# Kernel optimization log

Hardware: AMD Instinct MI355X
Metric: run time of the kernel (lower is better)

Reference implementation:

```python
import jax, jax.numpy as jnp
import numpy as np

N = 20000          # num_nodes
E = 160000         # directed edges (doubled to undirected inside reference)
NF, EF, H, OUT, K = 16, 16, 128, 16, 3


def mlp2(x, w1, b1, w2, b2):
    return jnp.maximum(x @ w1 + b1, 0.0) @ w2 + b2


def edge_agg(x, src, dst, eattr, w1, b1, w2, b2):
    # message = MLP(cat[x_i (target), x_j (source), edge_attr]); aggr='add' at target
    m = mlp2(jnp.concatenate([x[dst], x[src], eattr], axis=-1), w1, b1, w2, b2)
    return jax.ops.segment_sum(m, dst, num_segments=x.shape[0])


def tag_conv(x, src, dst, lins, bias):
    # PyG TAGConv: gcn_norm (no self loops), out = sum_k lin_k(L^k x) + bias
    n = x.shape[0]
    deg = jax.ops.segment_sum(jnp.ones_like(src, dtype=x.dtype), dst, num_segments=n)
    dis = jnp.where(deg > 0, jax.lax.rsqrt(deg), 0.0)
    norm = dis[src] * dis[dst]                     # [E]
    out = x @ lins[0]
    h = x
    for k in range(1, lins.shape[0]):
        h = jax.ops.segment_sum(norm[:, None] * h[src], dst, num_segments=n)
        out = out + h @ lins[k]
    return out + bias


def setup_inputs() -> dict:
    key = jax.random.key(0)
    ks = jax.random.split(key, 20)
    s = 0.05
    lin = lambda k, i, o: jax.random.normal(k, (i, o), jnp.float32) * s
    inp = {}
    inp["x"] = jax.random.normal(ks[0], (N, NF), jnp.float32)
    inp["mask"] = (jax.random.uniform(ks[1], (N, NF)) > 0.5).astype(jnp.float32)
    inp["edge_attr"] = jax.random.normal(ks[2], (E, EF), jnp.float32)
    inp["edge_index"] = jax.random.randint(ks[3], (2, E), 0, N)
    inp["m_w1"] = lin(ks[4], NF, H); inp["m_b1"] = jnp.zeros(H)
    inp["m_w2"] = lin(ks[5], H, NF); inp["m_b2"] = jnp.zeros(NF)
    inp["ea0_w1"] = lin(ks[6], 2 * NF + EF, H); inp["ea0_b1"] = jnp.zeros(H)
    inp["ea0_w2"] = lin(ks[7], H, H); inp["ea0_b2"] = jnp.zeros(H)
    inp["tag0_w"] = jax.random.normal(ks[8], (K + 1, H, H), jnp.float32) * s
    inp["tag0_b"] = jnp.zeros(H)
    inp["ea1_w1"] = lin(ks[9], 2 * H + EF, H); inp["ea1_b1"] = jnp.zeros(H)
    inp["ea1_w2"] = lin(ks[10], H, H); inp["ea1_b2"] = jnp.zeros(H)
    inp["tag1_w"] = jax.random.normal(ks[11], (K + 1, H, H), jnp.float32) * s
    inp["tag1_b"] = jnp.zeros(H)
    inp["ea2_w1"] = lin(ks[12], 2 * H + EF, H); inp["ea2_b1"] = jnp.zeros(H)
    inp["ea2_w2"] = lin(ks[13], H, OUT); inp["ea2_b2"] = jnp.zeros(OUT)
    return inp


def reference(x, mask, edge_attr, m_w1, m_b1, m_w2, m_b2,
              ea0_w1, ea0_b1, ea0_w2, ea0_b2, tag0_w, tag0_b,
              ea1_w1, ea1_b1, ea1_w2, ea1_b2, tag1_w, tag1_b,
              ea2_w1, ea2_b1, ea2_w2, ea2_b2, edge_index):
    # undirect_graph: random directed edges -> duplicate reversed copies
    src0, dst0 = edge_index[0], edge_index[1]
    src = jnp.concatenate([src0, dst0])
    dst = jnp.concatenate([dst0, src0])
    ea = jnp.concatenate([edge_attr, edge_attr], axis=0)
    # mask embedding + residual
    h = mlp2(mask, m_w1, m_b1, m_w2, m_b2) + x
    # [EA, TAG, EA, TAG] with ReLU (dropout = identity in eval)
    h = jnp.maximum(edge_agg(h, src, dst, ea, ea0_w1, ea0_b1, ea0_w2, ea0_b2), 0.0)
    h = jnp.maximum(tag_conv(h, src, dst, tag0_w, tag0_b), 0.0)
    h = jnp.maximum(edge_agg(h, src, dst, ea, ea1_w1, ea1_b1, ea1_w2, ea1_b2), 0.0)
    h = jnp.maximum(tag_conv(h, src, dst, tag1_w, tag1_b), 0.0)
    # final EA (no activation)
    return edge_agg(h, src, dst, ea, ea2_w1, ea2_b1, ea2_w2, ea2_b2)
```

## Files before the change

kernel.cpp:

```cpp
#include <hip/hip_runtime.h>

typedef unsigned short u16;
typedef unsigned int u32;

using bfrag  = __attribute__((ext_vector_type(8))) short;
using f32x4  = __attribute__((ext_vector_type(4))) float;
using f32x16 = __attribute__((ext_vector_type(16))) float;

__device__ __forceinline__ float b2f(u16 u) {
  union { u32 i; float f; } c; c.i = ((u32)u) << 16; return c.f;
}
__device__ __forceinline__ float bflo(u32 u) { union { u32 i; float f; } c; c.i = u << 16; return c.f; }
__device__ __forceinline__ float bfhi(u32 u) { union { u32 i; float f; } c; c.i = u & 0xffff0000u; return c.f; }
__device__ __forceinline__ u16 f2b(float f) {
  union { float f; u32 i; } c; c.f = f;
  u32 x = c.i;
  u32 r = x + 0x7fffu + ((x >> 16) & 1u);
  return (u16)(r >> 16);
}
__device__ __forceinline__ u32 packb2(float x, float y) {
  return ((u32)f2b(x)) | (((u32)f2b(y)) << 16);
}
__device__ __forceinline__ u16 f2h(float x) {
  union { _Float16 h; u16 u; } c; c.h = (_Float16)x; return c.u;
}
__device__ __forceinline__ float h2lo(u32 u) { union { u32 i; _Float16 h[2]; } c; c.i = u; return (float)c.h[0]; }
__device__ __forceinline__ float h2hi(u32 u) { union { u32 i; _Float16 h[2]; } c; c.i = u; return (float)c.h[1]; }
__device__ __forceinline__ int rfl(int v) { return __builtin_amdgcn_readfirstlane(v); }

__global__ __launch_bounds__(256) void count_deg(const int* __restrict__ eidx,
                                                 int* __restrict__ degi, int E) {
  int e = blockIdx.x * 256 + threadIdx.x;
  if (e >= E) return;
  atomicAdd(&degi[eidx[E + e]], 1);
  atomicAdd(&degi[eidx[e]], 1);
}

__global__ __launch_bounds__(256) void scan1(const int* __restrict__ degi,
                                             int* __restrict__ bsum, int N) {
  __shared__ int sh[256];
  int t = threadIdx.x;
  int gid = blockIdx.x * 256 + t;
  sh[t] = (gid < N) ? degi[gid] : 0;
  __syncthreads();
  for (int off = 128; off > 0; off >>= 1) {
    if (t < off) sh[t] += sh[t + off];
    __syncthreads();
  }
  if (t == 0) bsum[blockIdx.x] = sh[0];
}

__global__ __launch_bounds__(256) void scan2(int* __restrict__ bsum,
                                             int* __restrict__ rowptr, int nb, int N) {
  __shared__ int sh[256];
  int t = threadIdx.x;
  int v = (t < nb) ? bsum[t] : 0;
  sh[t] = v;
  __syncthreads();
  for (int off = 1; off < 256; off <<= 1) {
    int x = sh[t];
    int add = (t >= off) ? sh[t - off] : 0;
    __syncthreads();
    sh[t] = x + add;
    __syncthreads();
  }
  if (t < nb) bsum[t] = sh[t] - v;
  if (t == nb - 1) rowptr[N] = sh[t];
}

__global__ __launch_bounds__(256) void scan3(const int* __restrict__ degi,
                                             const int* __restrict__ bsum,
                                             int* __restrict__ rowptr,
                                             int* __restrict__ cursor,
                                             float* __restrict__ dis, int N) {
  __shared__ int sh[256];
  int t = threadIdx.x;
  int gid = blockIdx.x * 256 + t;
  int d = (gid < N) ? degi[gid] : 0;
  sh[t] = d;
  __syncthreads();
  for (int off = 1; off < 256; off <<= 1) {
    int x = sh[t];
    int add = (t >= off) ? sh[t - off] : 0;
    __syncthreads();
    sh[t] = x + add;
    __syncthreads();
  }
  if (gid < N) {
    int run = bsum[blockIdx.x] + sh[t] - d;
    rowptr[gid] = run;
    cursor[gid] = run;
    dis[gid] = d > 0 ? rsqrtf((float)d) : 0.0f;
  }
}

__global__ __launch_bounds__(256) void fill_csr(const int* __restrict__ eidx,
                                                int* __restrict__ cursor,
                                                const float* __restrict__ dis,
                                                int2* __restrict__ cw,
                                                int2* __restrict__ ce, int E) {
  int i = blockIdx.x * 256 + threadIdx.x;
  int E2 = 2 * E;
  if (i >= E2) return;
  int e = (i < E) ? i : i - E;
  int s, d;
  if (i < E) { s = eidx[e]; d = eidx[E + e]; }
  else       { s = eidx[E + e]; d = eidx[e]; }
  int pos = atomicAdd(&cursor[d], 1);
  cw[pos] = make_int2(s, __float_as_int(dis[s]));
  ce[pos] = make_int2(s, e);
}

__global__ __launch_bounds__(256) void prep_wt(
    const float* __restrict__ ea0_w2, const float* __restrict__ tag0_w,
    const float* __restrict__ ea1_w1, const float* __restrict__ ea1_w2,
    const float* __restrict__ tag1_w, const float* __restrict__ ea2_w1,
    const float* __restrict__ ea0_w1,
    u16* __restrict__ Wt, u16* __restrict__ W3, int* __restrict__ degi, int N) {
  int gid = blockIdx.x * 256 + threadIdx.x;
  if (gid < N) degi[gid] = 0;
  int t = threadIdx.x;
  if (blockIdx.x >= 112) {
    int tab = blockIdx.x - 112;
    const float* src = (tab == 0) ? (ea0_w1 + 32 * 128)
                     : (tab == 1) ? (ea1_w1 + 256 * 128)
                                  : (ea2_w1 + 256 * 128);
    u16* dst = W3 + tab * 2048;
    for (int i = 0; i < 8; ++i) {
      int idx = i * 256 + t;
      int n = idx >> 4, k = idx & 15;
      dst[idx] = f2b(src[k * 128 + n]);
    }
    return;
  }
  int mat = blockIdx.x >> 3, chunk = blockIdx.x & 7;
  const float* src;
  if      (mat == 0)  src = ea0_w2;
  else if (mat <= 4)  src = tag0_w + (mat - 1) * 16384;
  else if (mat == 5)  src = ea1_w1;
  else if (mat == 6)  src = ea1_w1 + 16384;
  else if (mat == 7)  src = ea1_w2;
  else if (mat <= 11) src = tag1_w + (mat - 8) * 16384;
  else if (mat == 12) src = ea2_w1;
  else                src = ea2_w1 + 16384;
  u16* dst = Wt + mat * 16384;
  for (int i = 0; i < 8; ++i) {
    int idx = chunk * 2048 + i * 256 + t;
    int k = idx >> 7, n = idx & 127;
    dst[n * 128 + k] = f2b(src[idx]);
  }
}

__global__ __launch_bounds__(256) void ea_proj_mfma(
    const float* __restrict__ ea, const u16* __restrict__ W3,
    u16* __restrict__ P0, u16* __restrict__ P1, u16* __restrict__ P2, int E) {
  __shared__ u16 Alds[64 * 16];
  __shared__ u16 Wlds[3 * 2048];
  int t = threadIdx.x;
  int base = blockIdx.x * 64;
  int rows = E - base; if (rows > 64) rows = 64;
#pragma unroll
  for (int i = 0; i < 3; ++i)
    *(uint4*)(Wlds + (i * 256 + t) * 8) = *(const uint4*)(W3 + (i * 256 + t) * 8);
#pragma unroll
  for (int i = 0; i < 4; ++i) {
    int idx = (i * 256 + t) * 4;
    float4 v = make_float4(0.f, 0.f, 0.f, 0.f);
    if ((idx >> 4) < rows) v = *(const float4*)(ea + (size_t)base * 16 + idx);
    ushort4 h;
    h.x = f2b(v.x); h.y = f2b(v.y); h.z = f2b(v.z); h.w = f2b(v.w);
    *(ushort4*)(Alds + idx) = h;
  }
  __syncthreads();
  int wave = t >> 6, lane = t & 63;
  int rowt = (wave >> 1) * 32;
  int colt = (wave & 1) * 64;
  int mm = lane & 31, kh = lane >> 5;
  bfrag a = *(const bfrag*)(Alds + (rowt + mm) * 16 + kh * 8);
#pragma unroll
  for (int tab = 0; tab < 3; ++tab) {
    const u16* wl = Wlds + tab * 2048;
    bfrag b0 = *(const bfrag*)(wl + (colt + mm) * 16 + kh * 8);
    bfrag b1 = *(const bfrag*)(wl + (colt + 32 + mm) * 16 + kh * 8);
    f32x16 acc0, acc1;
#pragma unroll
    for (int z = 0; z < 16; ++z) { acc0[z] = 0.f; acc1[z] = 0.f; }
    acc0 = __builtin_amdgcn_mfma_f32_32x32x16_bf16(a, b0, acc0, 0, 0, 0);
    acc1 = __builtin_amdgcn_mfma_f32_32x32x16_bf16(a, b1, acc1, 0, 0, 0);
    u16* P = (tab == 0) ? P0 : (tab == 1) ? P1 : P2;
#pragma unroll
    for (int reg = 0; reg < 16; ++reg) {
      int row = rowt + (reg & 3) + 8 * (reg >> 2) + 4 * kh;
      if (row < rows) {
        size_t off = (size_t)(base + row) * 128;
        P[off + colt + mm]      = f2h(acc0[reg]);
        P[off + colt + 32 + mm] = f2h(acc1[reg]);
      }
    }
  }
}

__global__ __launch_bounds__(128) void gemm_head(
    const float* __restrict__ mask, const float* __restrict__ x,
    const float* __restrict__ m_w1, const float* __restrict__ m_b1,
    const float* __restrict__ m_w2, const float* __restrict__ m_b2,
    const float* __restrict__ ea0_w1, const float* __restrict__ ea0_b1,
    u16* __restrict__ pb, u16* __restrict__ q, int M) {
  const int ROWS = 8;
  int t = threadIdx.x;
  int base = blockIdx.x * ROWS;
  __shared__ float Ml[ROWS * 16];
  __shared__ float T1[ROWS * 128];
  __shared__ float H[ROWS * 16];
  for (int i = t; i < ROWS * 16; i += 128) {
    int r = i >> 4, k = i & 15;
    int row = base + r;
    Ml[i] = (row < M) ? mask[(size_t)row * 16 + k] : 0.f;
  }
  __syncthreads();
  {
    float acc[ROWS];
#pragma unroll
    for (int r = 0; r < ROWS; ++r) acc[r] = m_b1[t];
    for (int k = 0; k < 16; ++k) {
      float w = m_w1[k * 128 + t];
#pragma unroll
      for (int r = 0; r < ROWS; ++r) acc[r] += Ml[r * 16 + k] * w;
    }
#pragma unroll
    for (int r = 0; r < ROWS; ++r) T1[r * 128 + t] = fmaxf(acc[r], 0.f);
  }
  __syncthreads();
  {
    int r = t >> 4, u = t & 15;
    float acc = m_b2[u];
    for (int k = 0; k < 128; ++k) acc += T1[r * 128 + k] * m_w2[k * 16 + u];
    int row = base + r;
    float xv = (row < M) ? x[(size_t)row * 16 + u] : 0.f;
    H[r * 16 + u] = acc + xv;
  }
  __syncthreads();
  {
    float aP[ROWS], aQ[ROWS];
    float b1v = ea0_b1[t];
#pragma unroll
    for (int r = 0; r < ROWS; ++r) { aP[r] = b1v; aQ[r] = 0.f; }
    for (int k = 0; k < 16; ++k) {
      float wd = ea0_w1[k * 128 + t];
      float ws = ea0_w1[(16 + k) * 128 + t];
#pragma unroll
      for (int r = 0; r < ROWS; ++r) {
        float h = H[r * 16 + k];
        aP[r] += h * wd;
        aQ[r] += h * ws;
      }
    }
#pragma unroll
    for (int r = 0; r < ROWS; ++r) {
      int row = base + r;
      if (row < M) {
        pb[(size_t)row * 128 + t] = f2b(aP[r]);
        q[(size_t)row * 128 + t]  = f2b(aQ[r]);
      }
    }
  }
}

template<bool OUTBF16>
__global__ __launch_bounds__(256) void gemm_mfma(
    const u16* __restrict__ A, const u16* __restrict__ Wt,
    void* __restrict__ Cout, const float* __restrict__ bias,
    const int* __restrict__ degi, int M, int relu) {
  __shared__ u16 Alds[64 * 136];
  __shared__ u16 Wlds[128 * 136];
  int t = threadIdx.x;
  int base = blockIdx.x * 64;
#pragma unroll
  for (int i = 0; i < 8; ++i) {
    int idx = (i * 256 + t) * 8;
    int n = idx >> 7, k = idx & 127;
    uint4 v = *(const uint4*)(Wt + idx);
    *(uint4*)(Wlds + n * 136 + k) = v;
  }
#pragma unroll
  for (int i = 0; i < 4; ++i) {
    int idx = (i * 256 + t) * 8;
    int r = idx >> 7, k = idx & 127;
    int row = base + r;
    uint4 v = make_uint4(0, 0, 0, 0);
    if (row < M) v = *(const uint4*)(A + (size_t)row * 128 + k);
    *(uint4*)(Alds + r * 136 + k) = v;
  }
  __syncthreads();
  int wave = t >> 6, lane = t & 63;
  int m = lane & 15, quad = lane >> 4;
  int arow = wave * 16 + m;
  bfrag a[4];
#pragma unroll
  for (int ks = 0; ks < 4; ++ks)
    a[ks] = *(const bfrag*)(Alds + arow * 136 + ks * 32 + quad * 8);
  f32x4 acc[8];
#pragma unroll
  for (int nt = 0; nt < 8; ++nt) acc[nt] = (f32x4){0.f, 0.f, 0.f, 0.f};
#pragma unroll
  for (int nt = 0; nt < 8; ++nt) {
    int n = nt * 16 + m;
#pragma unroll
    for (int ks = 0; ks < 4; ++ks) {
      bfrag b = *(const bfrag*)(Wlds + n * 136 + ks * 32 + quad * 8);
      acc[nt] = __builtin_amdgcn_mfma_f32_16x16x32_bf16(a[ks], b, acc[nt], 0, 0, 0);
    }
  }
#pragma unroll
  for (int nt = 0; nt < 8; ++nt) {
    int col = nt * 16 + m;
#pragma unroll
    for (int r = 0; r < 4; ++r) {
      int row = base + wave * 16 + quad * 4 + r;
      if (row < M) {
        float v = acc[nt][r];
        if (bias) { float b = bias[col]; v += degi ? b * (float)degi[row] : b; }
        if (relu) v = fmaxf(v, 0.f);
        if (OUTBF16) ((u16*)Cout)[(size_t)row * 128 + col] = f2b(v);
        else         ((float*)Cout)[(size_t)row * 128 + col] = v;
      }
    }
  }
}

__global__ __launch_bounds__(256) void gemm_mfma_dual(
    const u16* __restrict__ A, const u16* __restrict__ W0t, const u16* __restrict__ W1t,
    u16* __restrict__ C0, u16* __restrict__ C1, const float* __restrict__ bias0, int M) {
  __shared__ u16 Alds[64 * 136];
  __shared__ u16 Wlds[128 * 136];
  int t = threadIdx.x;
  int base = blockIdx.x * 64;
#pragma unroll
  for (int i = 0; i < 8; ++i) {
    int idx = (i * 256 + t) * 8;
    int n = idx >> 7, k = idx & 127;
    uint4 v = *(const uint4*)(W0t + idx);
    *(uint4*)(Wlds + n * 136 + k) = v;
  }
#pragma unroll
  for (int i = 0; i < 4; ++i) {
    int idx = (i * 256 + t) * 8;
    int r = idx >> 7, k = idx & 127;
    int row = base + r;
    uint4 v = make_uint4(0, 0, 0, 0);
    if (row < M) v = *(const uint4*)(A + (size_t)row * 128 + k);
    *(uint4*)(Alds + r * 136 + k) = v;
  }
  __syncthreads();
  int wave = t >> 6, lane = t & 63;
  int m = lane & 15, quad = lane >> 4;
  int arow = wave * 16 + m;
  bfrag a[4];
#pragma unroll
  for (int ks = 0; ks < 4; ++ks)
    a[ks] = *(const bfrag*)(Alds + arow * 136 + ks * 32 + quad * 8);
  f32x4 acc0[8], acc1[8];
#pragma unroll
  for (int nt = 0; nt < 8; ++nt) { acc0[nt] = (f32x4){0,0,0,0}; acc1[nt] = (f32x4){0,0,0,0}; }
#pragma unroll
  for (int nt = 0; nt < 8; ++nt) {
    int n = nt * 16 + m;
#pragma unroll
    for (int ks = 0; ks < 4; ++ks) {
      bfrag b = *(const bfrag*)(Wlds + n * 136 + ks * 32 + quad * 8);
      acc0[nt] = __builtin_amdgcn_mfma_f32_16x16x32_bf16(a[ks], b, acc0[nt], 0, 0, 0);
    }
  }
  __syncthreads();
#pragma unroll
  for (int i = 0; i < 8; ++i) {
    int idx = (i * 256 + t) * 8;
    int n = idx >> 7, k = idx & 127;
    uint4 v = *(const uint4*)(W1t + idx);
    *(uint4*)(Wlds + n * 136 + k) = v;
  }
  __syncthreads();
#pragma unroll
  for (int nt = 0; nt < 8; ++nt) {
    int n = nt * 16 + m;
#pragma unroll
    for (int ks = 0; ks < 4; ++ks) {
      bfrag b = *(const bfrag*)(Wlds + n * 136 + ks * 32 + quad * 8);
      acc1[nt] = __builtin_amdgcn_mfma_f32_16x16x32_bf16(a[ks], b, acc1[nt], 0, 0, 0);
    }
  }
#pragma unroll
  for (int nt = 0; nt < 8; ++nt) {
    int col = nt * 16 + m;
#pragma unroll
    for (int r = 0; r < 4; ++r) {
      int row = base + wave * 16 + quad * 4 + r;
      if (row < M) {
        float v0 = acc0[nt][r];
        if (bias0) v0 += bias0[col];
        C0[(size_t)row * 128 + col] = f2b(v0);
        C1[(size_t)row * 128 + col] = f2b(acc1[nt][r]);
      }
    }
  }
}

__global__ __launch_bounds__(256) void gemm_mfma_quad(
    const u16* __restrict__ A, const u16* __restrict__ Wt4,
    u16* __restrict__ G0, u16* __restrict__ G1,
    u16* __restrict__ G2, u16* __restrict__ G3, int M) {
  __shared__ u16 Alds[64 * 136];
  __shared__ u16 Wlds[128 * 136];
  int t = threadIdx.x;
  int base = blockIdx.x * 64;
#pragma unroll
  for (int i = 0; i < 4; ++i) {
    int idx = (i * 256 + t) * 8;
    int r = idx >> 7, k = idx & 127;
    int row = base + r;
    uint4 v = make_uint4(0, 0, 0, 0);
    if (row < M) v = *(const uint4*)(A + (size_t)row * 128 + k);
    *(uint4*)(Alds + r * 136 + k) = v;
  }
  __syncthreads();
  int wave = t >> 6, lane = t & 63;
  int m = lane & 15, quad = lane >> 4;
  int arow = wave * 16 + m;
  bfrag a[4];
#pragma unroll
  for (int ks = 0; ks < 4; ++ks)
    a[ks] = *(const bfrag*)(Alds + arow * 136 + ks * 32 + quad * 8);
#pragma unroll
  for (int mat = 0; mat < 4; ++mat) {
    __syncthreads();
#pragma unroll
    for (int i = 0; i < 8; ++i) {
      int idx = (i * 256 + t) * 8;
      int n = idx >> 7, k = idx & 127;
      uint4 v = *(const uint4*)(Wt4 + mat * 16384 + idx);
      *(uint4*)(Wlds + n * 136 + k) = v;
    }
    __syncthreads();
    f32x4 acc[8];
#pragma unroll
    for (int nt = 0; nt < 8; ++nt) acc[nt] = (f32x4){0.f, 0.f, 0.f, 0.f};
#pragma unroll
    for (int nt = 0; nt < 8; ++nt) {
      int n = nt * 16 + m;
#pragma unroll
      for (int ks = 0; ks < 4; ++ks) {
        bfrag b = *(const bfrag*)(Wlds + n * 136 + ks * 32 + quad * 8);
        acc[nt] = __builtin_amdgcn_mfma_f32_16x16x32_bf16(a[ks], b, acc[nt], 0, 0, 0);
      }
    }
    u16* G = (mat == 0) ? G0 : (mat == 1) ? G1 : (mat == 2) ? G2 : G3;
#pragma unroll
    for (int nt = 0; nt < 8; ++nt) {
      int col = nt * 16 + m;
#pragma unroll
      for (int r = 0; r < 4; ++r) {
        int row = base + wave * 16 + quad * 4 + r;
        if (row < M) G[(size_t)row * 128 + col] = f2b(acc[nt][r]);
      }
    }
  }
}

__global__ __launch_bounds__(128) void gemm_tail(
    const u16* __restrict__ A, const float* __restrict__ W, float* __restrict__ Cout,
    const float* __restrict__ bias, const int* __restrict__ degi, int M) {
  const int ROWS = 8;
  int t = threadIdx.x;
  int base = blockIdx.x * ROWS;
  __shared__ float Al[ROWS * 128];
  for (int i = t; i < ROWS * 128; i += 128) {
    int r = i >> 7, k = i & 127;
    int row = base + r;
    Al[i] = (row < M) ? b2f(A[(size_t)row * 128 + k]) : 0.f;
  }
  __syncthreads();
  int r = t >> 4, u = t & 15;
  int row = base + r;
  float acc = 0.f;
  for (int k = 0; k < 128; ++k) acc += Al[r * 128 + k] * W[k * 16 + u];
  if (row < M) {
    Cout[(size_t)row * 16 + u] = acc + bias[u] * (float)degi[row];
  }
}

__device__ __forceinline__ void tag_edge(const int2* __restrict__ rr, int j,
    const u16* __restrict__ g, int lane, float& x0, float& x1) {
  int2 r = rr[j];
  int s = rfl(r.x); float w = __uint_as_float(rfl(r.y));
  u32 h = *((const u32*)(g + (size_t)s * 128) + lane);
  x0 += w * bflo(h); x1 += w * bfhi(h);
}
__device__ __forceinline__ void ea_edge(const int2* __restrict__ rr, int j,
    const u16* __restrict__ q, const u16* __restrict__ P, int lane,
    float pb0, float pb1, float& x0, float& x1) {
  int2 r = rr[j];
  int s = rfl(r.x), i = rfl(r.y);
  u32 qv = *((const u32*)(q + (size_t)s * 128) + lane);
  u32 pv = *((const u32*)(P + (size_t)i * 128) + lane);
  x0 += fmaxf(pb0 + bflo(qv) + h2lo(pv), 0.f);
  x1 += fmaxf(pb1 + bfhi(qv) + h2hi(pv), 0.f);
}

template<bool FINAL>
__global__ __launch_bounds__(256) void tag_gather8(
    const u16* __restrict__ g, const u16* __restrict__ Cin,
    const float* __restrict__ bias, const float* __restrict__ dis,
    const int* __restrict__ rowptr, const int2* __restrict__ cw,
    u16* __restrict__ out, int N) {
  __shared__ int2 recs[4][64];
  int wave = threadIdx.x >> 6, lane = threadIdx.x & 63;
  int node = blockIdx.x * 4 + wave;
  if (node >= N) return;
  int e0 = rfl(rowptr[node]);
  int e1 = rfl(rowptr[node + 1]);
  int2* rr = recs[wave];
  float a0 = 0, a1 = 0, b0 = 0, b1 = 0;
  for (int base = e0; base < e1; base += 64) {
    if (base + lane < e1) rr[lane] = cw[base + lane];
    int cnt = min(64, e1 - base);
    int j = 0;
    for (; j + 8 <= cnt; j += 8) {
      tag_edge(rr, j + 0, g, lane, a0, a1);
      tag_edge(rr, j + 1, g, lane, b0, b1);
      tag_edge(rr, j + 2, g, lane, a0, a1);
      tag_edge(rr, j + 3, g, lane, b0, b1);
      tag_edge(rr, j + 4, g, lane, a0, a1);
      tag_edge(rr, j + 5, g, lane, b0, b1);
      tag_edge(rr, j + 6, g, lane, a0, a1);
      tag_edge(rr, j + 7, g, lane, b0, b1);
    }
    for (; j + 2 <= cnt; j += 2) {
      tag_edge(rr, j + 0, g, lane, a0, a1);
      tag_edge(rr, j + 1, g, lane, b0, b1);
    }
    if (j < cnt) tag_edge(rr, j, g, lane, a0, a1);
  }
  float dn = dis[node];
  float r0v = dn * (a0 + b0), r1v = dn * (a1 + b1);
  u32 cin = *((const u32*)(Cin + (size_t)node * 128) + lane);
  r0v += bflo(cin); r1v += bfhi(cin);
  if (FINAL) {
    float2 bv = *(const float2*)(bias + 2 * lane);
    r0v = fmaxf(r0v + bv.x, 0.f);
    r1v = fmaxf(r1v + bv.y, 0.f);
  }
  *((u32*)(out + (size_t)node * 128) + lane) = packb2(r0v, r1v);
}

__global__ __launch_bounds__(256) void ea_gather8(
    const u16* __restrict__ pb, const u16* __restrict__ q,
    const u16* __restrict__ P ,
    const int* __restrict__ rowptr, const int2* __restrict__ ce,
    u16* __restrict__ Hsum, int N) {
  __shared__ int2 recs[4][64];
  int wave = threadIdx.x >> 6, lane = threadIdx.x & 63;
  int node = blockIdx.x * 4 + wave;
  if (node >= N) return;
  int e0 = rfl(rowptr[node]);
  int e1 = rfl(rowptr[node + 1]);
  int2* rr = recs[wave];
  u32 pbu = *((const u32*)(pb + (size_t)node * 128) + lane);
  float pb0 = bflo(pbu), pb1 = bfhi(pbu);
  float a0 = 0, a1 = 0, b0 = 0, b1 = 0;
  for (int base = e0; base < e1; base += 64) {
    if (base + lane < e1) rr[lane] = ce[base + lane];
    int cnt = min(64, e1 - base);
    int j = 0;
    for (; j + 8 <= cnt; j += 8) {
      ea_edge(rr, j + 0, q, P, lane, pb0, pb1, a0, a1);
      ea_edge(rr, j + 1, q, P, lane, pb0, pb1, b0, b1);
      ea_edge(rr, j + 2, q, P, lane, pb0, pb1, a0, a1);
      ea_edge(rr, j + 3, q, P, lane, pb0, pb1, b0, b1);
      ea_edge(rr, j + 4, q, P, lane, pb0, pb1, a0, a1);
      ea_edge(rr, j + 5, q, P, lane, pb0, pb1, b0, b1);
      ea_edge(rr, j + 6, q, P, lane, pb0, pb1, a0, a1);
      ea_edge(rr, j + 7, q, P, lane, pb0, pb1, b0, b1);
    }
    for (; j + 2 <= cnt; j += 2) {
      ea_edge(rr, j + 0, q, P, lane, pb0, pb1, a0, a1);
      ea_edge(rr, j + 1, q, P, lane, pb0, pb1, b0, b1);
    }
    if (j < cnt) ea_edge(rr, j, q, P, lane, pb0, pb1, a0, a1);
  }
  *((u32*)(Hsum + (size_t)node * 128) + lane) = packb2(a0 + b0, a1 + b1);
}

extern "C" void kernel_launch(void* const* d_in, const int* in_sizes, int n_in,
                              void* d_out, int out_size, void* d_ws, size_t ws_size,
                              hipStream_t stream) {
  const float* x      = (const float*)d_in[0];
  const float* mask   = (const float*)d_in[1];
  const float* ea     = (const float*)d_in[2];
  const int*   eidx   = (const int*)d_in[3];
  const float* m_w1   = (const float*)d_in[4];
  const float* m_b1   = (const float*)d_in[5];
  const float* m_w2   = (const float*)d_in[6];
  const float* m_b2   = (const float*)d_in[7];
  const float* ea0_w1 = (const float*)d_in[8];
  const float* ea0_b1 = (const float*)d_in[9];
  const float* ea0_w2 = (const float*)d_in[10];
  const float* ea0_b2 = (const float*)d_in[11];
  const float* tag0_w = (const float*)d_in[12];
  const float* tag0_b = (const float*)d_in[13];
  const float* ea1_w1 = (const float*)d_in[14];
  const float* ea1_b1 = (const float*)d_in[15];
  const float* ea1_w2 = (const float*)d_in[16];
  const float* ea1_b2 = (const float*)d_in[17];
  const float* tag1_w = (const float*)d_in[18];
  const float* tag1_b = (const float*)d_in[19];
  const float* ea2_w1 = (const float*)d_in[20];
  const float* ea2_b1 = (const float*)d_in[21];
  const float* ea2_w2 = (const float*)d_in[22];
  const float* ea2_b2 = (const float*)d_in[23];

  const int N = in_sizes[0] / 16;
  const int E = in_sizes[2] / 16;
  const int E2 = 2 * E;
  const int NB = (N + 255) / 256;

  char* w = (char*)d_ws;
  auto alloc = [&](size_t bytes) { char* p = w; w += (bytes + 255) & ~(size_t)255; return p; };
  int*   degi   = (int*)alloc((size_t)N * 4);
  int*   cursor = (int*)alloc((size_t)N * 4);
  int*   rowptr = (int*)alloc((size_t)(N + 1) * 4);
  int*   bsum   = (int*)alloc((size_t)256 * 4);
  float* dis    = (float*)alloc((size_t)N * 4);
  int2*  cw     = (int2*)alloc((size_t)E2 * 8);
  int2*  ce     = (int2*)alloc((size_t)E2 * 8);
  u16*   X0     = (u16*)alloc((size_t)N * 128 * 2);
  u16*   X1     = (u16*)alloc((size_t)N * 128 * 2);
  u16*   X2     = (u16*)alloc((size_t)N * 128 * 2);
  u16*   G0     = (u16*)alloc((size_t)N * 128 * 2);
  u16*   G1     = (u16*)alloc((size_t)N * 128 * 2);
  u16*   G2     = (u16*)alloc((size_t)N * 128 * 2);
  u16*   G3     = (u16*)alloc((size_t)N * 128 * 2);
  u16*   Wt     = (u16*)alloc((size_t)14 * 16384 * 2);
  u16*   W3     = (u16*)alloc((size_t)3 * 2048 * 2);
  u16*   P0     = (u16*)alloc((size_t)E * 128 * 2);
  u16*   P1     = (u16*)alloc((size_t)E * 128 * 2);
  u16*   P2     = (u16*)alloc((size_t)E * 128 * 2);
  (void)ws_size; (void)n_in; (void)out_size;

  prep_wt<<<115, 256, 0, stream>>>(ea0_w2, tag0_w, ea1_w1, ea1_w2, tag1_w, ea2_w1,
                                   ea0_w1, Wt, W3, degi, N);
  ea_proj_mfma<<<(E + 63) / 64, 256, 0, stream>>>(ea, W3, P0, P1, P2, E);
  count_deg<<<(E + 255) / 256, 256, 0, stream>>>(eidx, degi, E);
  scan1<<<NB, 256, 0, stream>>>(degi, bsum, N);
  scan2<<<1, 256, 0, stream>>>(bsum, rowptr, NB, N);
  scan3<<<NB, 256, 0, stream>>>(degi, bsum, rowptr, cursor, dis, N);
  fill_csr<<<(E2 + 255) / 256, 256, 0, stream>>>(eidx, cursor, dis, cw, ce, E);

  const int gb = (N + 7) / 8;
  const int gm = (N + 63) / 64;
  const int g4 = (N + 3) / 4;
  u16* WT_ea0w2  = Wt + 0 * 16384;
  u16* WT_tag0   = Wt + 1 * 16384;
  u16* WT_ea1d   = Wt + 5 * 16384;
  u16* WT_ea1s   = Wt + 6 * 16384;
  u16* WT_ea1w2  = Wt + 7 * 16384;
  u16* WT_tag1   = Wt + 8 * 16384;
  u16* WT_ea2d   = Wt + 12 * 16384;
  u16* WT_ea2s   = Wt + 13 * 16384;

  gemm_head<<<gb, 128, 0, stream>>>(mask, x, m_w1, m_b1, m_w2, m_b2,
                                    ea0_w1, ea0_b1, X0, X1, N);

  ea_gather8<<<g4, 256, 0, stream>>>(X0, X1, P0, rowptr, ce, X2, N);
  gemm_mfma<true><<<gm, 256, 0, stream>>>(X2, WT_ea0w2, X0, ea0_b2, degi, N, 1);

  gemm_mfma_quad<<<gm, 256, 0, stream>>>(X0, WT_tag0, G0, G1, G2, G3, N);
  tag_gather8<false><<<g4, 256, 0, stream>>>(G3, G2, nullptr, dis, rowptr, cw, X1, N);
  tag_gather8<false><<<g4, 256, 0, stream>>>(X1, G1, nullptr, dis, rowptr, cw, X2, N);
  tag_gather8<true><<<g4, 256, 0, stream>>>(X2, G0, tag0_b, dis, rowptr, cw, X0, N);

  gemm_mfma_dual<<<gm, 256, 0, stream>>>(X0, WT_ea1d, WT_ea1s, X1, X2, ea1_b1, N);
  ea_gather8<<<g4, 256, 0, stream>>>(X1, X2, P1, rowptr, ce, G0, N);
  gemm_mfma<true><<<gm, 256, 0, stream>>>(G0, WT_ea1w2, X0, ea1_b2, degi, N, 1);

  gemm_mfma_quad<<<gm, 256, 0, stream>>>(X0, WT_tag1, G0, G1, G2, G3, N);
  tag_gather8<false><<<g4, 256, 0, stream>>>(G3, G2, nullptr, dis, rowptr, cw, X1, N);
  tag_gather8<false><<<g4, 256, 0, stream>>>(X1, G1, nullptr, dis, rowptr, cw, X2, N);
  tag_gather8<true><<<g4, 256, 0, stream>>>(X2, G0, tag1_b, dis, rowptr, cw, X0, N);

  gemm_mfma_dual<<<gm, 256, 0, stream>>>(X0, WT_ea2d, WT_ea2s, X1, X2, ea2_b1, N);
  ea_gather8<<<g4, 256, 0, stream>>>(X1, X2, P2, rowptr, ce, G0, N);
  gemm_tail<<<gb, 128, 0, stream>>>(G0, ea2_w2, (float*)d_out, ea2_b2, degi, N);
}
```

Measured before the change: 429.4 us.

## Fuse prologue kernels and merge EA second-layer GEMM into TAG quad GEMM

Merges weight prep, edge-attr projection and degree counting into one prologue launch, merges CSR fill with the head MLP, and fuses the EA w2 GEMM (bias×degree, ReLU) into the TAG four-way GEMM via LDS. The aim is fewer kernel launches and no round trip of the intermediate node features through global memory. In the second penta call G0 is both input and output, which can race across blocks only if tiles overlap. Each block reads its own rows before writing, so it looks safe.

```diff
diff --git a/kernel.cpp b/kernel.cpp
--- a/kernel.cpp
+++ b/kernel.cpp
@@ -28,112 +28,78 @@
 __device__ __forceinline__ float h2hi(u32 u) { union { u32 i; _Float16 h[2]; } c; c.i = u; return (float)c.h[1]; }
 __device__ __forceinline__ int rfl(int v) { return __builtin_amdgcn_readfirstlane(v); }
 
-__global__ __launch_bounds__(256) void count_deg(const int* __restrict__ eidx,
-                                                 int* __restrict__ degi, int E) {
-  int e = blockIdx.x * 256 + threadIdx.x;
-  if (e >= E) return;
-  atomicAdd(&degi[eidx[E + e]], 1);
-  atomicAdd(&degi[eidx[e]], 1);
-}
-
-__global__ __launch_bounds__(256) void scan1(const int* __restrict__ degi,
-                                             int* __restrict__ bsum, int N) {
-  __shared__ int sh[256];
-  int t = threadIdx.x;
-  int gid = blockIdx.x * 256 + t;
-  sh[t] = (gid < N) ? degi[gid] : 0;
-  __syncthreads();
-  for (int off = 128; off > 0; off >>= 1) {
-    if (t < off) sh[t] += sh[t + off];
-    __syncthreads();
-  }
-  if (t == 0) bsum[blockIdx.x] = sh[0];
-}
-
-__global__ __launch_bounds__(256) void scan2(int* __restrict__ bsum,
-                                             int* __restrict__ rowptr, int nb, int N) {
-  __shared__ int sh[256];
-  int t = threadIdx.x;
-  int v = (t < nb) ? bsum[t] : 0;
-  sh[t] = v;
-  __syncthreads();
-  for (int off = 1; off < 256; off <<= 1) {
-    int x = sh[t];
-    int add = (t >= off) ? sh[t - off] : 0;
-    __syncthreads();
-    sh[t] = x + add;
-    __syncthreads();
-  }
-  if (t < nb) bsum[t] = sh[t] - v;
-  if (t == nb - 1) rowptr[N] = sh[t];
-}
-
-__global__ __launch_bounds__(256) void scan3(const int* __restrict__ degi,
-                                             const int* __restrict__ bsum,
-                                             int* __restrict__ rowptr,
-                                             int* __restrict__ cursor,
-                                             float* __restrict__ dis, int N) {
-  __shared__ int sh[256];
-  int t = threadIdx.x;
-  int gid = blockIdx.x * 256 + t;
-  int d = (gid < N) ? degi[gid] : 0;
-  sh[t] = d;
-  __syncthreads();
-  for (int off = 1; off < 256; off <<= 1) {
-    int x = sh[t];
-    int add = (t >= off) ? sh[t - off] : 0;
-    __syncthreads();
-    sh[t] = x + add;
-    __syncthreads();
-  }
-  if (gid < N) {
-    int run = bsum[blockIdx.x] + sh[t] - d;
-    rowptr[gid] = run;
-    cursor[gid] = run;
-    dis[gid] = d > 0 ? rsqrtf((float)d) : 0.0f;
-  }
-}
-
-__global__ __launch_bounds__(256) void fill_csr(const int* __restrict__ eidx,
-                                                int* __restrict__ cursor,
-                                                const float* __restrict__ dis,
-                                                int2* __restrict__ cw,
-                                                int2* __restrict__ ce, int E) {
-  int i = blockIdx.x * 256 + threadIdx.x;
-  int E2 = 2 * E;
-  if (i >= E2) return;
-  int e = (i < E) ? i : i - E;
-  int s, d;
-  if (i < E) { s = eidx[e]; d = eidx[E + e]; }
-  else       { s = eidx[E + e]; d = eidx[e]; }
-  int pos = atomicAdd(&cursor[d], 1);
-  cw[pos] = make_int2(s, __float_as_int(dis[s]));
-  ce[pos] = make_int2(s, e);
-}
-
-__global__ __launch_bounds__(256) void prep_wt(
-    const float* __restrict__ ea0_w2, const float* __restrict__ tag0_w,
-    const float* __restrict__ ea1_w1, const float* __restrict__ ea1_w2,
-    const float* __restrict__ tag1_w, const float* __restrict__ ea2_w1,
-    const float* __restrict__ ea0_w1,
-    u16* __restrict__ Wt, u16* __restrict__ W3, int* __restrict__ degi, int N) {
-  int gid = blockIdx.x * 256 + threadIdx.x;
-  if (gid < N) degi[gid] = 0;
-  int t = threadIdx.x;
-  if (blockIdx.x >= 112) {
-    int tab = blockIdx.x - 112;
-    const float* src = (tab == 0) ? (ea0_w1 + 32 * 128)
-                     : (tab == 1) ? (ea1_w1 + 256 * 128)
-                                  : (ea2_w1 + 256 * 128);
-    u16* dst = W3 + tab * 2048;
+__global__ __launch_bounds__(256) void prologue(
+    const float* __restrict__ ea, const int* __restrict__ eidx,
+    const float* __restrict__ ea0_w1, const float* __restrict__ ea0_w2,
+    const float* __restrict__ tag0_w, const float* __restrict__ ea1_w1,
+    const float* __restrict__ ea1_w2, const float* __restrict__ tag1_w,
+    const float* __restrict__ ea2_w1,
+    u16* __restrict__ P0, u16* __restrict__ P1, u16* __restrict__ P2,
+    int* __restrict__ degi, u16* __restrict__ Wt, int E, int N,
+    int PB, int CB) {
+  int t = threadIdx.x;
+  if (blockIdx.x < (unsigned)PB) {
+    __shared__ u16 Alds[64 * 16];
+    __shared__ u16 Wlds[3 * 2048];
+    int base = blockIdx.x * 64;
+    int rows = E - base; if (rows > 64) rows = 64;
+    const float* wsrc[3] = { ea0_w1 + 32 * 128, ea1_w1 + 256 * 128, ea2_w1 + 256 * 128 };
+#pragma unroll
     for (int i = 0; i < 8; ++i) {
       int idx = i * 256 + t;
       int n = idx >> 4, k = idx & 15;
-      dst[idx] = f2b(src[k * 128 + n]);
+      Wlds[0 * 2048 + idx] = f2b(wsrc[0][k * 128 + n]);
+      Wlds[1 * 2048 + idx] = f2b(wsrc[1][k * 128 + n]);
+      Wlds[2 * 2048 + idx] = f2b(wsrc[2][k * 128 + n]);
+    }
+#pragma unroll
+    for (int i = 0; i < 4; ++i) {
+      int idx = (i * 256 + t) * 4;
+      float4 v = make_float4(0.f, 0.f, 0.f, 0.f);
+      if ((idx >> 4) < rows) v = *(const float4*)(ea + (size_t)base * 16 + idx);
+      ushort4 h;
+      h.x = f2b(v.x); h.y = f2b(v.y); h.z = f2b(v.z); h.w = f2b(v.w);
+      *(ushort4*)(Alds + idx) = h;
+    }
+    __syncthreads();
+    int wave = t >> 6, lane = t & 63;
+    int rowt = (wave >> 1) * 32;
+    int colt = (wave & 1) * 64;
+    int mm = lane & 31, kh = lane >> 5;
+    bfrag a = *(const bfrag*)(Alds + (rowt + mm) * 16 + kh * 8);
+#pragma unroll
+    for (int tab = 0; tab < 3; ++tab) {
+      const u16* wl = Wlds + tab * 2048;
+      bfrag b0 = *(const bfrag*)(wl + (colt + mm) * 16 + kh * 8);
+      bfrag b1 = *(const bfrag*)(wl + (colt + 32 + mm) * 16 + kh * 8);
+      f32x16 acc0, acc1;
+#pragma unroll
+      for (int z = 0; z < 16; ++z) { acc0[z] = 0.f; acc1[z] = 0.f; }
+      acc0 = __builtin_amdgcn_mfma_f32_32x32x16_bf16(a, b0, acc0, 0, 0, 0);
+      acc1 = __builtin_amdgcn_mfma_f32_32x32x16_bf16(a, b1, acc1, 0, 0, 0);
+      u16* P = (tab == 0) ? P0 : (tab == 1) ? P1 : P2;
+#pragma unroll
+      for (int reg = 0; reg < 16; ++reg) {
+        int row = rowt + (reg & 3) + 8 * (reg >> 2) + 4 * kh;
+        if (row < rows) {
+          size_t off = (size_t)(base + row) * 128;
+          P[off + colt + mm]      = f2h(acc0[reg]);
+          P[off + colt + 32 + mm] = f2h(acc1[reg]);
+        }
+      }
     }
     return;
   }
-  int mat = blockIdx.x >> 3, chunk = blockIdx.x & 7;
+  if (blockIdx.x < (unsigned)(PB + CB)) {
+    int e = (blockIdx.x - PB) * 256 + t;
+    if (e < E) {
+      atomicAdd(&degi[eidx[E + e]], 1);
+      atomicAdd(&degi[eidx[e]], 1);
+    }
+    return;
+  }
+  int wb = blockIdx.x - PB - CB;
+  int mat = wb >> 3, chunk = wb & 7;
   const float* src;
   if      (mat == 0)  src = ea0_w2;
   else if (mat <= 4)  src = tag0_w + (mat - 1) * 16384;
@@ -151,84 +117,109 @@
   }
 }
 
-__global__ __launch_bounds__(256) void ea_proj_mfma(
-    const float* __restrict__ ea, const u16* __restrict__ W3,
-    u16* __restrict__ P0, u16* __restrict__ P1, u16* __restrict__ P2, int E) {
-  __shared__ u16 Alds[64 * 16];
-  __shared__ u16 Wlds[3 * 2048];
-  int t = threadIdx.x;
-  int base = blockIdx.x * 64;
-  int rows = E - base; if (rows > 64) rows = 64;
-#pragma unroll
-  for (int i = 0; i < 3; ++i)
-    *(uint4*)(Wlds + (i * 256 + t) * 8) = *(const uint4*)(W3 + (i * 256 + t) * 8);
-#pragma unroll
-  for (int i = 0; i < 4; ++i) {
-    int idx = (i * 256 + t) * 4;
-    float4 v = make_float4(0.f, 0.f, 0.f, 0.f);
-    if ((idx >> 4) < rows) v = *(const float4*)(ea + (size_t)base * 16 + idx);
-    ushort4 h;
-    h.x = f2b(v.x); h.y = f2b(v.y); h.z = f2b(v.z); h.w = f2b(v.w);
-    *(ushort4*)(Alds + idx) = h;
-  }
-  __syncthreads();
-  int wave = t >> 6, lane = t & 63;
-  int rowt = (wave >> 1) * 32;
-  int colt = (wave & 1) * 64;
-  int mm = lane & 31, kh = lane >> 5;
-  bfrag a = *(const bfrag*)(Alds + (rowt + mm) * 16 + kh * 8);
-#pragma unroll
-  for (int tab = 0; tab < 3; ++tab) {
-    const u16* wl = Wlds + tab * 2048;
-    bfrag b0 = *(const bfrag*)(wl + (colt + mm) * 16 + kh * 8);
-    bfrag b1 = *(const bfrag*)(wl + (colt + 32 + mm) * 16 + kh * 8);
-    f32x16 acc0, acc1;
-#pragma unroll
-    for (int z = 0; z < 16; ++z) { acc0[z] = 0.f; acc1[z] = 0.f; }
-    acc0 = __builtin_amdgcn_mfma_f32_32x32x16_bf16(a, b0, acc0, 0, 0, 0);
-    acc1 = __builtin_amdgcn_mfma_f32_32x32x16_bf16(a, b1, acc1, 0, 0, 0);
-    u16* P = (tab == 0) ? P0 : (tab == 1) ? P1 : P2;
-#pragma unroll
-    for (int reg = 0; reg < 16; ++reg) {
-      int row = rowt + (reg & 3) + 8 * (reg >> 2) + 4 * kh;
-      if (row < rows) {
-        size_t off = (size_t)(base + row) * 128;
-        P[off + colt + mm]      = f2h(acc0[reg]);
-        P[off + colt + 32 + mm] = f2h(acc1[reg]);
-      }
-    }
-  }
-}
-
-__global__ __launch_bounds__(128) void gemm_head(
+__global__ __launch_bounds__(256) void scan1(const int* __restrict__ degi,
+                                             int* __restrict__ bsum, int N) {
+  __shared__ int sh[256];
+  int t = threadIdx.x;
+  int gid = blockIdx.x * 256 + t;
+  sh[t] = (gid < N) ? degi[gid] : 0;
+  __syncthreads();
+  for (int off = 128; off > 0; off >>= 1) {
+    if (t < off) sh[t] += sh[t + off];
+    __syncthreads();
+  }
+  if (t == 0) bsum[blockIdx.x] = sh[0];
+}
+
+__global__ __launch_bounds__(256) void scan2(int* __restrict__ bsum,
+                                             int* __restrict__ rowptr, int nb, int N) {
+  __shared__ int sh[256];
+  int t = threadIdx.x;
+  int v = (t < nb) ? bsum[t] : 0;
+  sh[t] = v;
+  __syncthreads();
+  for (int off = 1; off < 256; off <<= 1) {
+    int x = sh[t];
+    int add = (t >= off) ? sh[t - off] : 0;
+    __syncthreads();
+    sh[t] = x + add;
+    __syncthreads();
+  }
+  if (t < nb) bsum[t] = sh[t] - v;
+  if (t == nb - 1) rowptr[N] = sh[t];
+}
+
+__global__ __launch_bounds__(256) void scan3(const int* __restrict__ degi,
+                                             const int* __restrict__ bsum,
+                                             int* __restrict__ rowptr,
+                                             int* __restrict__ cursor,
+                                             float* __restrict__ dis, int N) {
+  __shared__ int sh[256];
+  int t = threadIdx.x;
+  int gid = blockIdx.x * 256 + t;
+  int d = (gid < N) ? degi[gid] : 0;
+  sh[t] = d;
+  __syncthreads();
+  for (int off = 1; off < 256; off <<= 1) {
+    int x = sh[t];
+    int add = (t >= off) ? sh[t - off] : 0;
+    __syncthreads();
+    sh[t] = x + add;
+    __syncthreads();
+  }
+  if (gid < N) {
+    int run = bsum[blockIdx.x] + sh[t] - d;
+    rowptr[gid] = run;
+    cursor[gid] = run;
+    dis[gid] = d > 0 ? rsqrtf((float)d) : 0.0f;
+  }
+}
+
+__global__ __launch_bounds__(256) void fill_head(
+    const int* __restrict__ eidx, int* __restrict__ cursor,
+    const float* __restrict__ dis, int2* __restrict__ cw, int2* __restrict__ ce, int E,
     const float* __restrict__ mask, const float* __restrict__ x,
     const float* __restrict__ m_w1, const float* __restrict__ m_b1,
     const float* __restrict__ m_w2, const float* __restrict__ m_b2,
     const float* __restrict__ ea0_w1, const float* __restrict__ ea0_b1,
-    u16* __restrict__ pb, u16* __restrict__ q, int M) {
-  const int ROWS = 8;
-  int t = threadIdx.x;
-  int base = blockIdx.x * ROWS;
-  __shared__ float Ml[ROWS * 16];
-  __shared__ float T1[ROWS * 128];
-  __shared__ float H[ROWS * 16];
-  for (int i = t; i < ROWS * 16; i += 128) {
-    int r = i >> 4, k = i & 15;
+    u16* __restrict__ pb, u16* __restrict__ q, int M, int FB) {
+  int t = threadIdx.x;
+  if (blockIdx.x < (unsigned)FB) {
+    int i = blockIdx.x * 256 + t;
+    int E2 = 2 * E;
+    if (i >= E2) return;
+    int e = (i < E) ? i : i - E;
+    int s, d;
+    if (i < E) { s = eidx[e]; d = eidx[E + e]; }
+    else       { s = eidx[E + e]; d = eidx[e]; }
+    int pos = atomicAdd(&cursor[d], 1);
+    cw[pos] = make_int2(s, __float_as_int(dis[s]));
+    ce[pos] = make_int2(s, e);
+    return;
+  }
+  __shared__ float Ml[16 * 16];
+  __shared__ float T1[16 * 128];
+  __shared__ float H[16 * 16];
+  int base = (blockIdx.x - FB) * 16;
+  {
+    int r = t >> 4, k = t & 15;
     int row = base + r;
-    Ml[i] = (row < M) ? mask[(size_t)row * 16 + k] : 0.f;
+    Ml[t] = (row < M) ? mask[(size_t)row * 16 + k] : 0.f;
   }
   __syncthreads();
   {
-    float acc[ROWS];
-#pragma unroll
-    for (int r = 0; r < ROWS; ++r) acc[r] = m_b1[t];
+    int col = t & 127, h2 = t >> 7;
+    float acc[8];
+    float b1v = m_b1[col];
+#pragma unroll
+    for (int r = 0; r < 8; ++r) acc[r] = b1v;
     for (int k = 0; k < 16; ++k) {
-      float w = m_w1[k * 128 + t];
-#pragma unroll
-      for (int r = 0; r < ROWS; ++r) acc[r] += Ml[r * 16 + k] * w;
-    }
-#pragma unroll
-    for (int r = 0; r < ROWS; ++r) T1[r * 128 + t] = fmaxf(acc[r], 0.f);
+      float w = m_w1[k * 128 + col];
+#pragma unroll
+      for (int r = 0; r < 8; ++r) acc[r] += Ml[(h2 * 8 + r) * 16 + k] * w;
+    }
+#pragma unroll
+    for (int r = 0; r < 8; ++r) T1[(h2 * 8 + r) * 128 + col] = fmaxf(acc[r], 0.f);
   }
   __syncthreads();
   {
@@ -237,30 +228,31 @@
     for (int k = 0; k < 128; ++k) acc += T1[r * 128 + k] * m_w2[k * 16 + u];
     int row = base + r;
     float xv = (row < M) ? x[(size_t)row * 16 + u] : 0.f;
-    H[r * 16 + u] = acc + xv;
+    H[t] = acc + xv;
   }
   __syncthreads();
   {
-    float aP[ROWS], aQ[ROWS];
-    float b1v = ea0_b1[t];
-#pragma unroll
-    for (int r = 0; r < ROWS; ++r) { aP[r] = b1v; aQ[r] = 0.f; }
+    int col = t & 127, h2 = t >> 7;
+    float aP[8], aQ[8];
+    float b1v = ea0_b1[col];
+#pragma unroll
+    for (int r = 0; r < 8; ++r) { aP[r] = b1v; aQ[r] = 0.f; }
     for (int k = 0; k < 16; ++k) {
-      float wd = ea0_w1[k * 128 + t];
-      float ws = ea0_w1[(16 + k) * 128 + t];
-#pragma unroll
-      for (int r = 0; r < ROWS; ++r) {
-        float h = H[r * 16 + k];
+      float wd = ea0_w1[k * 128 + col];
+      float ws = ea0_w1[(16 + k) * 128 + col];
+#pragma unroll
+      for (int r = 0; r < 8; ++r) {
+        float h = H[(h2 * 8 + r) * 16 + k];
         aP[r] += h * wd;
         aQ[r] += h * ws;
       }
     }
 #pragma unroll
-    for (int r = 0; r < ROWS; ++r) {
-      int row = base + r;
+    for (int r = 0; r < 8; ++r) {
+      int row = base + h2 * 8 + r;
       if (row < M) {
-        pb[(size_t)row * 128 + t] = f2b(aP[r]);
-        q[(size_t)row * 128 + t]  = f2b(aQ[r]);
+        pb[(size_t)row * 128 + col] = f2b(aP[r]);
+        q[(size_t)row * 128 + col]  = f2b(aQ[r]);
       }
     }
   }
@@ -405,14 +397,22 @@
   }
 }
 
-__global__ __launch_bounds__(256) void gemm_mfma_quad(
-    const u16* __restrict__ A, const u16* __restrict__ Wt4,
+__global__ __launch_bounds__(256) void gemm_mfma_penta(
+    const u16* __restrict__ A, const u16* __restrict__ W2t, const u16* __restrict__ Wt4,
+    const float* __restrict__ bias, const int* __restrict__ degi,
     u16* __restrict__ G0, u16* __restrict__ G1,
     u16* __restrict__ G2, u16* __restrict__ G3, int M) {
   __shared__ u16 Alds[64 * 136];
   __shared__ u16 Wlds[128 * 136];
   int t = threadIdx.x;
   int base = blockIdx.x * 64;
+#pragma unroll
+  for (int i = 0; i < 8; ++i) {
+    int idx = (i * 256 + t) * 8;
+    int n = idx >> 7, k = idx & 127;
+    uint4 v = *(const uint4*)(W2t + idx);
+    *(uint4*)(Wlds + n * 136 + k) = v;
+  }
 #pragma unroll
   for (int i = 0; i < 4; ++i) {
     int idx = (i * 256 + t) * 8;
@@ -427,6 +427,35 @@
   int m = lane & 15, quad = lane >> 4;
   int arow = wave * 16 + m;
   bfrag a[4];
+#pragma unroll
+  for (int ks = 0; ks < 4; ++ks)
+    a[ks] = *(const bfrag*)(Alds + arow * 136 + ks * 32 + quad * 8);
+  {
+    f32x4 acc[8];
+#pragma unroll
+    for (int nt = 0; nt < 8; ++nt) acc[nt] = (f32x4){0.f, 0.f, 0.f, 0.f};
+#pragma unroll
+    for (int nt = 0; nt < 8; ++nt) {
+      int n = nt * 16 + m;
+#pragma unroll
+      for (int ks = 0; ks < 4; ++ks) {
+        bfrag b = *(const bfrag*)(Wlds + n * 136 + ks * 32 + quad * 8);
+        acc[nt] = __builtin_amdgcn_mfma_f32_16x16x32_bf16(a[ks], b, acc[nt], 0, 0, 0);
+      }
+    }
+#pragma unroll
+    for (int nt = 0; nt < 8; ++nt) {
+      int col = nt * 16 + m;
+#pragma unroll
+      for (int r = 0; r < 4; ++r) {
+        int lrow = wave * 16 + quad * 4 + r;
+        int row = base + lrow;
+        float v = 0.f;
+        if (row < M) v = fmaxf(acc[nt][r] + bias[col] * (float)degi[row], 0.f);
+        Alds[lrow * 136 + col] = f2b(v);
+      }
+    }
+  }
 #pragma unroll
   for (int ks = 0; ks < 4; ++ks)
     a[ks] = *(const bfrag*)(Alds + arow * 136 + ks * 32 + quad * 8);
@@ -640,24 +669,19 @@
   u16*   G2     = (u16*)alloc((size_t)N * 128 * 2);
   u16*   G3     = (u16*)alloc((size_t)N * 128 * 2);
   u16*   Wt     = (u16*)alloc((size_t)14 * 16384 * 2);
-  u16*   W3     = (u16*)alloc((size_t)3 * 2048 * 2);
   u16*   P0     = (u16*)alloc((size_t)E * 128 * 2);
   u16*   P1     = (u16*)alloc((size_t)E * 128 * 2);
   u16*   P2     = (u16*)alloc((size_t)E * 128 * 2);
   (void)ws_size; (void)n_in; (void)out_size;
 
-  prep_wt<<<115, 256, 0, stream>>>(ea0_w2, tag0_w, ea1_w1, ea1_w2, tag1_w, ea2_w1,
-                                   ea0_w1, Wt, W3, degi, N);
-  ea_proj_mfma<<<(E + 63) / 64, 256, 0, stream>>>(ea, W3, P0, P1, P2, E);
-  count_deg<<<(E + 255) / 256, 256, 0, stream>>>(eidx, degi, E);
-  scan1<<<NB, 256, 0, stream>>>(degi, bsum, N);
-  scan2<<<1, 256, 0, stream>>>(bsum, rowptr, NB, N);
-  scan3<<<NB, 256, 0, stream>>>(degi, bsum, rowptr, cursor, dis, N);
-  fill_csr<<<(E2 + 255) / 256, 256, 0, stream>>>(eidx, cursor, dis, cw, ce, E);
-
-  const int gb = (N + 7) / 8;
+  const int PB = (E + 63) / 64;
+  const int CB = (E + 255) / 256;
+  const int FB = (E2 + 255) / 256;
+  const int HB = (N + 15) / 16;
   const int gm = (N + 63) / 64;
   const int g4 = (N + 3) / 4;
+  const int gb = (N + 7) / 8;
+
   u16* WT_ea0w2  = Wt + 0 * 16384;
   u16* WT_tag0   = Wt + 1 * 16384;
   u16* WT_ea1d   = Wt + 5 * 16384;
@@ -667,22 +691,28 @@
   u16* WT_ea2d   = Wt + 12 * 16384;
   u16* WT_ea2s   = Wt + 13 * 16384;
 
-  gemm_head<<<gb, 128, 0, stream>>>(mask, x, m_w1, m_b1, m_w2, m_b2,
-                                    ea0_w1, ea0_b1, X0, X1, N);
+  hipMemsetAsync(degi, 0, (size_t)N * 4, stream);
+  prologue<<<PB + CB + 112, 256, 0, stream>>>(ea, eidx, ea0_w1, ea0_w2, tag0_w,
+                                              ea1_w1, ea1_w2, tag1_w, ea2_w1,
+                                              P0, P1, P2, degi, Wt, E, N, PB, CB);
+  scan1<<<NB, 256, 0, stream>>>(degi, bsum, N);
+  scan2<<<1, 256, 0, stream>>>(bsum, rowptr, NB, N);
+  scan3<<<NB, 256, 0, stream>>>(degi, bsum, rowptr, cursor, dis, N);
+  fill_head<<<FB + HB, 256, 0, stream>>>(eidx, cursor, dis, cw, ce, E,
+                                         mask, x, m_w1, m_b1, m_w2, m_b2,
+                                         ea0_w1, ea0_b1, X0, X1, N, FB);
 
   ea_gather8<<<g4, 256, 0, stream>>>(X0, X1, P0, rowptr, ce, X2, N);
-  gemm_mfma<true><<<gm, 256, 0, stream>>>(X2, WT_ea0w2, X0, ea0_b2, degi, N, 1);
-
-  gemm_mfma_quad<<<gm, 256, 0, stream>>>(X0, WT_tag0, G0, G1, G2, G3, N);
+  gemm_mfma_penta<<<gm, 256, 0, stream>>>(X2, WT_ea0w2, WT_tag0, ea0_b2, degi,
+                                          G0, G1, G2, G3, N);
   tag_gather8<false><<<g4, 256, 0, stream>>>(G3, G2, nullptr, dis, rowptr, cw, X1, N);
   tag_gather8<false><<<g4, 256, 0, stream>>>(X1, G1, nullptr, dis, rowptr, cw, X2, N);
   tag_gather8<true><<<g4, 256, 0, stream>>>(X2, G0, tag0_b, dis, rowptr, cw, X0, N);
 
   gemm_mfma_dual<<<gm, 256, 0, stream>>>(X0, WT_ea1d, WT_ea1s, X1, X2, ea1_b1, N);
   ea_gather8<<<g4, 256, 0, stream>>>(X1, X2, P1, rowptr, ce, G0, N);
-  gemm_mfma<true><<<gm, 256, 0, stream>>>(G0, WT_ea1w2, X0, ea1_b2, degi, N, 1);
-
-  gemm_mfma_quad<<<gm, 256, 0, stream>>>(X0, WT_tag1, G0, G1, G2, G3, N);
+  gemm_mfma_penta<<<gm, 256, 0, stream>>>(G0, WT_ea1w2, WT_tag1, ea1_b2, degi,
+                                          G0, G1, G2, G3, N);
   tag_gather8<false><<<g4, 256, 0, stream>>>(G3, G2, nullptr, dis, rowptr, cw, X1, N);
   tag_gather8<false><<<g4, 256, 0, stream>>>(X1, G1, nullptr, dis, rowptr, cw, X2, N);
   tag_gather8<true><<<g4, 256, 0, stream>>>(X2, G0, tag1_b, dis, rowptr, cw, X0, N);
```

Measured after the change: 424.5 us. About the same (-1.1%).
